# Kernel optimization log

Hardware: AMD Instinct MI355X
Metric: run time of the kernel (lower is better)

## Reference

```python
import jax, jax.numpy as jnp
import numpy as np

N_NODES = 50000
N_EDGES = 800000
FEAT = 128
HID = 64
N_CLS = 12


def setup_inputs() -> dict:
    key = jax.random.key(0)
    ks = jax.random.split(key, 8)
    x = jax.random.normal(ks[0], (N_NODES, FEAT), dtype=jnp.float32)
    edge_index = jax.random.randint(ks[1], (2, N_EDGES), 0, N_NODES, dtype=jnp.int64)
    s1 = 1.0 / np.sqrt(FEAT)
    s2 = 1.0 / np.sqrt(HID)
    W1 = jax.random.uniform(ks[2], (FEAT, HID), jnp.float32, -s1, s1)
    b1 = jnp.zeros((HID,), jnp.float32)
    W2 = jax.random.uniform(ks[3], (HID, HID), jnp.float32, -s2, s2)
    b2 = jnp.zeros((HID,), jnp.float32)
    Wfc = jax.random.uniform(ks[4], (HID, N_CLS), jnp.float32, -s2, s2)
    bfc = jax.random.uniform(ks[5], (N_CLS,), jnp.float32, -s2, s2)
    return {"x": x, "edge_index": edge_index, "W1": W1, "b1": b1,
            "W2": W2, "b2": b2, "Wfc": Wfc, "bfc": bfc}


def gcn_conv(x, W, b, src, dst, n_nodes):
    """PyG GCNConv: symmetric-normalized aggregation with self-loops.
    out_i = sum_{j in N(i)} (xW)_j / sqrt(d_i d_j) + (xW)_i / d_i + b,
    where d = in-degree + 1 (self loop)."""
    xw = x @ W  # [N, out] -- transform before propagate (PyG order)
    deg = jnp.zeros((n_nodes,), x.dtype).at[dst].add(1.0) + 1.0
    dinv = jax.lax.rsqrt(deg)
    norm = dinv[src] * dinv[dst]  # [E]
    agg = jax.ops.segment_sum(xw[src] * norm[:, None], dst, num_segments=n_nodes)
    agg = agg + xw * (dinv * dinv)[:, None]  # self-loop term
    return agg + b


def reference(x, edge_index, W1, b1, W2, b2, Wfc, bfc):
    n = x.shape[0]
    src, dst = edge_index[0], edge_index[1]
    h = jax.nn.relu(gcn_conv(x, W1, b1, src, dst, n))
    h = jax.nn.relu(gcn_conv(h, W2, b2, src, dst, n))
    return h @ Wfc + bfc  # [N, num_content_categories]
```

## Files before the change

kernel.cpp:

```cpp
#include <hip/hip_runtime.h>
#include <hip/hip_fp16.h>


#define CAP   64
#define NBUK  196
#define ET    4096
#define BCAP  5120

typedef unsigned short u16;
typedef unsigned long long u64;
typedef _Float16 f16;
typedef _Float16 f16x8 __attribute__((ext_vector_type(8)));
typedef float f32x4 __attribute__((ext_vector_type(4)));

__global__ __launch_bounds__(256) void k_prep(const float* __restrict__ W1,
                                              const float* __restrict__ W2,
                                              f16* __restrict__ W1t,
                                              f16* __restrict__ W2t,
                                              int* __restrict__ gcur) {
    int i = blockIdx.x * 256 + threadIdx.x;
    if (i < NBUK) gcur[i] = 0;
    if (i < 128 * 64) {
        int k = i >> 6, nn = i & 63;
        W1t[nn * 128 + k] = (f16)W1[k * 64 + nn];
    }
    int j = i - 128 * 64;
    if (j >= 0 && j < 64 * 64) {
        int k = j >> 6, nn = j & 63;
        W2t[nn * 64 + k] = (f16)W2[k * 64 + nn];
    }
}

__global__ __launch_bounds__(256) void k_scat(const int* __restrict__ src,
                                              const int* __restrict__ dst,
                                              int* __restrict__ gcur,
                                              unsigned* __restrict__ eb, int E) {
    __shared__ int hist[NBUK];
    __shared__ int cur[NBUK];
    const int tid = threadIdx.x, blk = blockIdx.x;
    for (int i = tid; i < NBUK; i += 256) hist[i] = 0;
    __syncthreads();

    const int e0 = blk * ET;
    unsigned pk[16];
    if (e0 + ET <= E) {
        const int4* s4 = (const int4*)(src + e0);
        const int4* d4 = (const int4*)(dst + e0);
#pragma unroll
        for (int j = 0; j < ET / 1024; j++) {
            int4 sv = s4[j * 256 + tid];
            int4 dv = d4[j * 256 + tid];
            pk[4 * j + 0] = ((unsigned)dv.x << 16) | (unsigned)sv.x;
            pk[4 * j + 1] = ((unsigned)dv.y << 16) | (unsigned)sv.y;
            pk[4 * j + 2] = ((unsigned)dv.z << 16) | (unsigned)sv.z;
            pk[4 * j + 3] = ((unsigned)dv.w << 16) | (unsigned)sv.w;
            atomicAdd(&hist[(unsigned)dv.x >> 8], 1);
            atomicAdd(&hist[(unsigned)dv.y >> 8], 1);
            atomicAdd(&hist[(unsigned)dv.z >> 8], 1);
            atomicAdd(&hist[(unsigned)dv.w >> 8], 1);
        }
    } else {
#pragma unroll
        for (int j = 0; j < ET / 256; j++) {
            int e = e0 + j * 256 + tid;
            unsigned u = 0xffffffffu;
            if (e < E) {
                unsigned d = (unsigned)dst[e];
                u = (d << 16) | (unsigned)src[e];
                atomicAdd(&hist[d >> 8], 1);
            }
            pk[j] = u;
        }
    }
    __syncthreads();
    for (int b = tid; b < NBUK; b += 256)
        cur[b] = b * BCAP + atomicAdd(&gcur[b], hist[b]);
    __syncthreads();
#pragma unroll
    for (int j = 0; j < 16; j++) {
        unsigned u = pk[j];
        if (u != 0xffffffffu) eb[atomicAdd(&cur[u >> 24], 1)] = u;
    }
}

__global__ __launch_bounds__(1024) void k_buildb(const unsigned* __restrict__ eb,
                                                 const int* __restrict__ gcur,
                                                 u16* __restrict__ csr,
                                                 int* __restrict__ cnt, int n) {
    __shared__ u16 lcsr[256 * CAP];
    __shared__ int cur[256];
    const int tid = threadIdx.x, b = blockIdx.x;
    if (tid < 256) cur[tid] = 0;
    __syncthreads();
    const int e0 = b * BCAP, e1 = e0 + gcur[b];
    for (int e = e0 + tid; e < e1; e += 1024) {
        unsigned u = __builtin_nontemporal_load(eb + e);
        int ld = (int)((u >> 16) & 255u);
        int p = atomicAdd(&cur[ld], 1);
        if (p < CAP) lcsr[ld * CAP + p] = (u16)(u & 0xffffu);
    }
    __syncthreads();
    const int node0 = b * 256;
    for (int i = tid; i < 256 * CAP / 8; i += 1024) {
        int r = i / (CAP / 8), q = i % (CAP / 8);
        int c = cur[r] < CAP ? cur[r] : CAP;
        uint4 v = *(uint4*)&lcsr[r * CAP + q * 8];
        if (q * 8 >= c) v = make_uint4(0, 0, 0, 0);
        *(uint4*)&csr[(size_t)(node0 + r) * CAP + q * 8] = v;
    }
    if (tid < 256 && node0 + tid < n) cnt[node0 + tid] = cur[tid];
}

template <int K, bool IS_HALF, typename TIN>
__global__ __launch_bounds__(256) void k_gemm(const TIN* __restrict__ X,
                                              const f16* __restrict__ Wt,
                                              const int* __restrict__ cnt,
                                              __half* __restrict__ Y, int n) {
    constexpr int KS = K + 8;
    __shared__ f16 xsh[64 * KS];
    __shared__ f16 wsh[64 * KS];
    const int tid = threadIdx.x;
    const int row0 = blockIdx.x * 64;

    for (int i = tid; i < 64 * (K / 8); i += 256) {
        int nn = i / (K / 8), kq = i % (K / 8);
        *(uint4*)&wsh[nn * KS + 8 * kq] = *(const uint4*)&Wt[nn * K + 8 * kq];
    }
    if constexpr (IS_HALF) {
        const __half* Xh = (const __half*)X;
        for (int i = tid; i < 64 * (K / 8); i += 256) {
            int r = i / (K / 8), kq = i % (K / 8);
            uint4 u = make_uint4(0, 0, 0, 0);
            int row = row0 + r;
            if (row < n) u = *(const uint4*)&Xh[(size_t)row * K + 8 * kq];
            *(uint4*)&xsh[r * KS + 8 * kq] = u;
        }
    } else {
        const float* Xf = (const float*)X;
        for (int i = tid; i < 64 * (K / 4); i += 256) {
            int r = i / (K / 4), q4 = i % (K / 4);
            float4 v = make_float4(0.f, 0.f, 0.f, 0.f);
            int row = row0 + r;
            if (row < n) v = *(const float4*)&Xf[(size_t)row * K + 4 * q4];
            __half2 p0 = __floats2half2_rn(v.x, v.y);
            __half2 p1 = __floats2half2_rn(v.z, v.w);
            uint2 o = make_uint2(*(unsigned*)&p0, *(unsigned*)&p1);
            *(uint2*)&xsh[r * KS + 4 * q4] = o;
        }
    }
    __syncthreads();

    const int wv = tid >> 6;
    const int lane = tid & 63;
    const int mn = lane & 15;
    const int q = lane >> 4;

    f32x4 acc[4] = {{0, 0, 0, 0}, {0, 0, 0, 0}, {0, 0, 0, 0}, {0, 0, 0, 0}};
    const f16* arow = &xsh[(16 * wv + mn) * KS + 8 * q];
#pragma unroll
    for (int s = 0; s < K / 32; s++) {
        f16x8 A = *(const f16x8*)&arow[32 * s];
#pragma unroll
        for (int c = 0; c < 4; c++) {
            f16x8 B = *(const f16x8*)&wsh[(16 * c + mn) * KS + 32 * s + 8 * q];
            acc[c] = __builtin_amdgcn_mfma_f32_16x16x32_f16(A, B, acc[c], 0, 0, 0);
        }
    }

    const int rowb = row0 + 16 * wv + 4 * q;
    float dinv[4];
#pragma unroll
    for (int r = 0; r < 4; r++)
        dinv[r] = rsqrtf((float)((rowb + r < n) ? cnt[rowb + r] : 0) + 1.0f);
#pragma unroll
    for (int c = 0; c < 4; c++)
#pragma unroll
        for (int r = 0; r < 4; r++) {
            int row = rowb + r;
            if (row < n)
                Y[(size_t)row * 64 + 16 * c + mn] = __float2half(acc[c][r] * dinv[r]);
        }
}

__device__ __forceinline__ float4 gather_node(const __half* __restrict__ y,
                                              const u16* __restrict__ lst,
                                              int deg, int c4) {
    float4 a0 = make_float4(0.f, 0.f, 0.f, 0.f);
    float4 a1 = make_float4(0.f, 0.f, 0.f, 0.f);
    int i = 0;
    for (; i + 16 <= deg; i += 16) {
        const u64* lp = (const u64*)(lst + i);
        u64 q0 = __builtin_nontemporal_load(lp);
        u64 q1 = __builtin_nontemporal_load(lp + 1);
        u64 q2 = __builtin_nontemporal_load(lp + 2);
        u64 q3 = __builtin_nontemporal_load(lp + 3);
        unsigned idx[16];
#pragma unroll
        for (int t = 0; t < 4; t++) {
            idx[t]      = (unsigned)((q0 >> (16 * t)) & 0xffffu);
            idx[t + 4]  = (unsigned)((q1 >> (16 * t)) & 0xffffu);
            idx[t + 8]  = (unsigned)((q2 >> (16 * t)) & 0xffffu);
            idx[t + 12] = (unsigned)((q3 >> (16 * t)) & 0xffffu);
        }
        uint2 v[16];
#pragma unroll
        for (int t = 0; t < 16; t++) v[t] = *(const uint2*)&y[(size_t)idx[t] * 64 + 4 * c4];
#pragma unroll
        for (int t = 0; t < 16; t += 2) {
            float2 lo0 = __half22float2(*(__half2*)&v[t].x);
            float2 hi0 = __half22float2(*(__half2*)&v[t].y);
            float2 lo1 = __half22float2(*(__half2*)&v[t + 1].x);
            float2 hi1 = __half22float2(*(__half2*)&v[t + 1].y);
            a0.x += lo0.x; a0.y += lo0.y; a0.z += hi0.x; a0.w += hi0.y;
            a1.x += lo1.x; a1.y += lo1.y; a1.z += hi1.x; a1.w += hi1.y;
        }
    }
    if (i + 8 <= deg) {
        const u64* lp = (const u64*)(lst + i);
        u64 q0 = __builtin_nontemporal_load(lp);
        u64 q1 = __builtin_nontemporal_load(lp + 1);
        unsigned idx[8];
#pragma unroll
        for (int t = 0; t < 4; t++) {
            idx[t]     = (unsigned)((q0 >> (16 * t)) & 0xffffu);
            idx[t + 4] = (unsigned)((q1 >> (16 * t)) & 0xffffu);
        }
        uint2 v[8];
#pragma unroll
        for (int t = 0; t < 8; t++) v[t] = *(const uint2*)&y[(size_t)idx[t] * 64 + 4 * c4];
#pragma unroll
        for (int t = 0; t < 8; t += 2) {
            float2 lo0 = __half22float2(*(__half2*)&v[t].x);
            float2 hi0 = __half22float2(*(__half2*)&v[t].y);
            float2 lo1 = __half22float2(*(__half2*)&v[t + 1].x);
            float2 hi1 = __half22float2(*(__half2*)&v[t + 1].y);
            a0.x += lo0.x; a0.y += lo0.y; a0.z += hi0.x; a0.w += hi0.y;
            a1.x += lo1.x; a1.y += lo1.y; a1.z += hi1.x; a1.w += hi1.y;
        }
        i += 8;
    }
    if (i + 4 <= deg) {
        u64 q0 = __builtin_nontemporal_load((const u64*)(lst + i));
        unsigned idx[4];
#pragma unroll
        for (int t = 0; t < 4; t++) idx[t] = (unsigned)((q0 >> (16 * t)) & 0xffffu);
        uint2 v[4];
#pragma unroll
        for (int t = 0; t < 4; t++) v[t] = *(const uint2*)&y[(size_t)idx[t] * 64 + 4 * c4];
#pragma unroll
        for (int t = 0; t < 4; t += 2) {
            float2 lo0 = __half22float2(*(__half2*)&v[t].x);
            float2 hi0 = __half22float2(*(__half2*)&v[t].y);
            float2 lo1 = __half22float2(*(__half2*)&v[t + 1].x);
            float2 hi1 = __half22float2(*(__half2*)&v[t + 1].y);
            a0.x += lo0.x; a0.y += lo0.y; a0.z += hi0.x; a0.w += hi0.y;
            a1.x += lo1.x; a1.y += lo1.y; a1.z += hi1.x; a1.w += hi1.y;
        }
        i += 4;
    }
    for (; i < deg; i++) {
        uint2 vv = *(const uint2*)&y[(size_t)lst[i] * 64 + 4 * c4];
        float2 lo = __half22float2(*(__half2*)&vv.x);
        float2 hi = __half22float2(*(__half2*)&vv.y);
        a0.x += lo.x; a0.y += lo.y; a0.z += hi.x; a0.w += hi.y;
    }
    return make_float4(a0.x + a1.x, a0.y + a1.y, a0.z + a1.z, a0.w + a1.w);
}

__global__ __launch_bounds__(256) void k_agg1(const __half* __restrict__ y,
                                              const u16* __restrict__ csr,
                                              const int* __restrict__ cnt,
                                              const float* __restrict__ bias,
                                              __half* __restrict__ h1, int n) {
    const int tid = threadIdx.x;
    const int c4 = tid & 15;
    const int node = blockIdx.x * 16 + (tid >> 4);
    if (node >= n) return;
    int deg_raw = cnt[node];
    int deg = deg_raw > CAP ? CAP : deg_raw;
    float4 acc = gather_node(y, csr + node * CAP, deg, c4);
    uint2 sv = *(const uint2*)&y[(size_t)node * 64 + 4 * c4];
    float2 slo = __half22float2(*(__half2*)&sv.x);
    float2 shi = __half22float2(*(__half2*)&sv.y);
    float d = rsqrtf((float)deg_raw + 1.0f);
    float4 bv = *(const float4*)&bias[4 * c4];
    float v0 = fmaxf(fmaf(d, acc.x + slo.x, bv.x), 0.f);
    float v1 = fmaxf(fmaf(d, acc.y + slo.y, bv.y), 0.f);
    float v2 = fmaxf(fmaf(d, acc.z + shi.x, bv.z), 0.f);
    float v3 = fmaxf(fmaf(d, acc.w + shi.y, bv.w), 0.f);
    __half2 o0 = __floats2half2_rn(v0, v1);
    __half2 o1 = __floats2half2_rn(v2, v3);
    u64 packed = (u64)(*(unsigned*)&o0) | ((u64)(*(unsigned*)&o1) << 32);
    __builtin_nontemporal_store(packed, (u64*)&h1[(size_t)node * 64 + 4 * c4]);
}

__global__ __launch_bounds__(256) void k_agg2fc(const __half* __restrict__ y,
                                                const u16* __restrict__ csr,
                                                const int* __restrict__ cnt,
                                                const float* __restrict__ bias,
                                                const float* __restrict__ Wfc,
                                                const float* __restrict__ bfc,
                                                float* __restrict__ out, int n) {
    __shared__ float wf[12 * 64];
    __shared__ float bf[12];
    const int tid = threadIdx.x;
    for (int i = tid; i < 12 * 64; i += 256) {
        int c = i >> 6, k = i & 63;
        wf[i] = Wfc[k * 12 + c];
    }
    if (tid < 12) bf[tid] = bfc[tid];
    __syncthreads();

    const int c4 = tid & 15;
    const int node = blockIdx.x * 16 + (tid >> 4);
    if (node >= n) return;
    int deg_raw = cnt[node];
    int deg = deg_raw > CAP ? CAP : deg_raw;
    float4 acc = gather_node(y, csr + node * CAP, deg, c4);
    uint2 sv = *(const uint2*)&y[(size_t)node * 64 + 4 * c4];
    float2 slo = __half22float2(*(__half2*)&sv.x);
    float2 shi = __half22float2(*(__half2*)&sv.y);
    float d = rsqrtf((float)deg_raw + 1.0f);
    float4 bv = *(const float4*)&bias[4 * c4];
    float v0 = fmaxf(fmaf(d, acc.x + slo.x, bv.x), 0.f);
    float v1 = fmaxf(fmaf(d, acc.y + slo.y, bv.y), 0.f);
    float v2 = fmaxf(fmaf(d, acc.z + shi.x, bv.z), 0.f);
    float v3 = fmaxf(fmaf(d, acc.w + shi.y, bv.w), 0.f);

    float res = 0.f;
#pragma unroll
    for (int c = 0; c < 12; c++) {
        float4 wv = *(const float4*)&wf[c * 64 + 4 * c4];
        float p = v0 * wv.x + v1 * wv.y + v2 * wv.z + v3 * wv.w;
        p += __shfl_xor(p, 1);
        p += __shfl_xor(p, 2);
        p += __shfl_xor(p, 4);
        p += __shfl_xor(p, 8);
        if (c4 == c) res = p + bf[c];
    }
    if (c4 < 12) out[(size_t)node * 12 + c4] = res;
}

extern "C" void kernel_launch(void* const* d_in, const int* in_sizes, int n_in,
                              void* d_out, int out_size, void* d_ws, size_t ws_size,
                              hipStream_t stream) {
    const float* x   = (const float*)d_in[0];
    const int*   ei  = (const int*)d_in[1];
    const float* W1  = (const float*)d_in[2];
    const float* b1  = (const float*)d_in[3];
    const float* W2  = (const float*)d_in[4];
    const float* b2  = (const float*)d_in[5];
    const float* Wfc = (const float*)d_in[6];
    const float* bfc = (const float*)d_in[7];
    float* out = (float*)d_out;

    const int n = in_sizes[0] / 128;
    const int E = in_sizes[1] / 2;
    const int* src = ei;
    const int* dst = ei + E;
    const int nblk = (E + ET - 1) / ET;

    char* w = (char*)d_ws;
    unsigned* eb  = (unsigned*)w;  w += (size_t)NBUK * BCAP * 4;
    int* gcur     = (int*)w;       w += 256 * 4;
    int* cnt      = (int*)w;       w += (size_t)((n + 63) / 64) * 64 * 4;
    f16* W1t      = (f16*)w;       w += 128 * 64 * 2;
    f16* W2t      = (f16*)w;       w += 64 * 64 * 2 + 256;
    u16* csr      = (u16*)w;       w += (size_t)NBUK * 256 * CAP * 2;
    __half* y     = (__half*)w;    w += (size_t)n * 64 * 2;
    __half* h1    = (__half*)w;

    k_prep   <<<dim3(48), dim3(256), 0, stream>>>(W1, W2, W1t, W2t, gcur);
    k_scat   <<<dim3(nblk), dim3(256), 0, stream>>>(src, dst, gcur, eb, E);
    k_buildb <<<dim3(NBUK), dim3(1024), 0, stream>>>(eb, gcur, csr, cnt, n);
    k_gemm<128, false, float><<<dim3((n + 63) / 64), dim3(256), 0, stream>>>(x, W1t, cnt, y, n);
    k_agg1   <<<dim3((n + 15) / 16), dim3(256), 0, stream>>>(y, csr, cnt, b1, h1, n);
    k_gemm<64, true, __half><<<dim3((n + 63) / 64), dim3(256), 0, stream>>>(h1, W2t, cnt, y, n);
    k_agg2fc <<<dim3((n + 15) / 16), dim3(256), 0, stream>>>(y, csr, cnt, b2, Wfc, bfc, out, n);
}
```

Baseline: 164.6 us.

## Fuse layer-1 aggregation with layer-2 GEMM via per-block MFMA

Merges the first aggregation kernel and the second dense transform into one kernel. Each block aggregates 16 nodes into shared memory, then uses MFMA 16x16x32 f16 instructions against W2 staged in LDS to produce the scaled layer-2 features directly. This removes the h1 intermediate write/read round trip and one kernel launch. In exchange, every block reloads W2 into LDS, uses more shared memory, and adds a block-wide barrier that could lower occupancy.

```diff
diff --git a/kernel.cpp b/kernel.cpp
--- a/kernel.cpp
+++ b/kernel.cpp
@@ -267,12 +267,84 @@
     return make_float4(a0.x + a1.x, a0.y + a1.y, a0.z + a1.z, a0.w + a1.w);
 }
 
-__global__ __launch_bounds__(256) void k_agg1(const __half* __restrict__ y,
-                                              const u16* __restrict__ csr,
-                                              const int* __restrict__ cnt,
-                                              const float* __restrict__ bias,
-                                              __half* __restrict__ h1, int n) {
+__global__ __launch_bounds__(256) void k_agg1g2(const __half* __restrict__ y,
+                                                const u16* __restrict__ csr,
+                                                const int* __restrict__ cnt,
+                                                const float* __restrict__ bias,
+                                                const f16* __restrict__ W2t,
+                                                __half* __restrict__ y2, int n) {
+    constexpr int KS2 = 64 + 8;
+    __shared__ f16 ash[16 * KS2];
+    __shared__ f16 wsh[64 * KS2];
+    __shared__ float dsh[16];
     const int tid = threadIdx.x;
+    const int node0 = blockIdx.x * 16;
+
+    for (int i = tid; i < 64 * 8; i += 256) {
+        int nn = i >> 3, kq = i & 7;
+        *(uint4*)&wsh[nn * KS2 + 8 * kq] = *(const uint4*)&W2t[nn * 64 + 8 * kq];
+    }
+
+    const int c4 = tid & 15;
+    const int r16 = tid >> 4;
+    const int node = node0 + r16;
+    const int nodeC = node < n ? node : 0;
+    int deg_raw = (node < n) ? cnt[node] : 0;
+    int deg = deg_raw > CAP ? CAP : deg_raw;
+    float4 acc = gather_node(y, csr + (size_t)nodeC * CAP, deg, c4);
+    uint2 sv = *(const uint2*)&y[(size_t)nodeC * 64 + 4 * c4];
+    float2 slo = __half22float2(*(__half2*)&sv.x);
+    float2 shi = __half22float2(*(__half2*)&sv.y);
+    float d = rsqrtf((float)deg_raw + 1.0f);
+    float4 bv = *(const float4*)&bias[4 * c4];
+    float v0 = fmaxf(fmaf(d, acc.x + slo.x, bv.x), 0.f);
+    float v1 = fmaxf(fmaf(d, acc.y + slo.y, bv.y), 0.f);
+    float v2 = fmaxf(fmaf(d, acc.z + shi.x, bv.z), 0.f);
+    float v3 = fmaxf(fmaf(d, acc.w + shi.y, bv.w), 0.f);
+    __half2 o0 = __floats2half2_rn(v0, v1);
+    __half2 o1 = __floats2half2_rn(v2, v3);
+    u64 packed = (u64)(*(unsigned*)&o0) | ((u64)(*(unsigned*)&o1) << 32);
+    *(u64*)&ash[r16 * KS2 + 4 * c4] = packed;
+    if (c4 == 0) dsh[r16] = d;
+    __syncthreads();
+
+    const int wv = tid >> 6;
+    const int lane = tid & 63;
+    const int mn = lane & 15;
+    const int q = lane >> 4;
+    f32x4 acc2 = {0, 0, 0, 0};
+#pragma unroll
+    for (int s = 0; s < 2; s++) {
+        f16x8 A = *(const f16x8*)&ash[mn * KS2 + 32 * s + 8 * q];
+        f16x8 B = *(const f16x8*)&wsh[(16 * wv + mn) * KS2 + 32 * s + 8 * q];
+        acc2 = __builtin_amdgcn_mfma_f32_16x16x32_f16(A, B, acc2, 0, 0, 0);
+    }
+#pragma unroll
+    for (int r = 0; r < 4; r++) {
+        int row = node0 + 4 * q + r;
+        if (row < n)
+            y2[(size_t)row * 64 + 16 * wv + mn] =
+                __float2half(acc2[r] * dsh[4 * q + r]);
+    }
+}
+
+__global__ __launch_bounds__(256) void k_agg2fc(const __half* __restrict__ y,
+                                                const u16* __restrict__ csr,
+                                                const int* __restrict__ cnt,
+                                                const float* __restrict__ bias,
+                                                const float* __restrict__ Wfc,
+                                                const float* __restrict__ bfc,
+                                                float* __restrict__ out, int n) {
+    __shared__ float wf[12 * 64];
+    __shared__ float bf[12];
+    const int tid = threadIdx.x;
+    for (int i = tid; i < 12 * 64; i += 256) {
+        int c = i >> 6, k = i & 63;
+        wf[i] = Wfc[k * 12 + c];
+    }
+    if (tid < 12) bf[tid] = bfc[tid];
+    __syncthreads();
+
     const int c4 = tid & 15;
     const int node = blockIdx.x * 16 + (tid >> 4);
     if (node >= n) return;
@@ -288,44 +360,6 @@
     float v1 = fmaxf(fmaf(d, acc.y + slo.y, bv.y), 0.f);
     float v2 = fmaxf(fmaf(d, acc.z + shi.x, bv.z), 0.f);
     float v3 = fmaxf(fmaf(d, acc.w + shi.y, bv.w), 0.f);
-    __half2 o0 = __floats2half2_rn(v0, v1);
-    __half2 o1 = __floats2half2_rn(v2, v3);
-    u64 packed = (u64)(*(unsigned*)&o0) | ((u64)(*(unsigned*)&o1) << 32);
-    __builtin_nontemporal_store(packed, (u64*)&h1[(size_t)node * 64 + 4 * c4]);
-}
-
-__global__ __launch_bounds__(256) void k_agg2fc(const __half* __restrict__ y,
-                                                const u16* __restrict__ csr,
-                                                const int* __restrict__ cnt,
-                                                const float* __restrict__ bias,
-                                                const float* __restrict__ Wfc,
-                                                const float* __restrict__ bfc,
-                                                float* __restrict__ out, int n) {
-    __shared__ float wf[12 * 64];
-    __shared__ float bf[12];
-    const int tid = threadIdx.x;
-    for (int i = tid; i < 12 * 64; i += 256) {
-        int c = i >> 6, k = i & 63;
-        wf[i] = Wfc[k * 12 + c];
-    }
-    if (tid < 12) bf[tid] = bfc[tid];
-    __syncthreads();
-
-    const int c4 = tid & 15;
-    const int node = blockIdx.x * 16 + (tid >> 4);
-    if (node >= n) return;
-    int deg_raw = cnt[node];
-    int deg = deg_raw > CAP ? CAP : deg_raw;
-    float4 acc = gather_node(y, csr + node * CAP, deg, c4);
-    uint2 sv = *(const uint2*)&y[(size_t)node * 64 + 4 * c4];
-    float2 slo = __half22float2(*(__half2*)&sv.x);
-    float2 shi = __half22float2(*(__half2*)&sv.y);
-    float d = rsqrtf((float)deg_raw + 1.0f);
-    float4 bv = *(const float4*)&bias[4 * c4];
-    float v0 = fmaxf(fmaf(d, acc.x + slo.x, bv.x), 0.f);
-    float v1 = fmaxf(fmaf(d, acc.y + slo.y, bv.y), 0.f);
-    float v2 = fmaxf(fmaf(d, acc.z + shi.x, bv.z), 0.f);
-    float v3 = fmaxf(fmaf(d, acc.w + shi.y, bv.w), 0.f);
 
     float res = 0.f;
 #pragma unroll
@@ -368,13 +402,12 @@
     f16* W2t      = (f16*)w;       w += 64 * 64 * 2 + 256;
     u16* csr      = (u16*)w;       w += (size_t)NBUK * 256 * CAP * 2;
     __half* y     = (__half*)w;    w += (size_t)n * 64 * 2;
-    __half* h1    = (__half*)w;
+    __half* y2    = (__half*)w;
 
     k_prep   <<<dim3(48), dim3(256), 0, stream>>>(W1, W2, W1t, W2t, gcur);
     k_scat   <<<dim3(nblk), dim3(256), 0, stream>>>(src, dst, gcur, eb, E);
     k_buildb <<<dim3(NBUK), dim3(1024), 0, stream>>>(eb, gcur, csr, cnt, n);
     k_gemm<128, false, float><<<dim3((n + 63) / 64), dim3(256), 0, stream>>>(x, W1t, cnt, y, n);
-    k_agg1   <<<dim3((n + 15) / 16), dim3(256), 0, stream>>>(y, csr, cnt, b1, h1, n);
-    k_gemm<64, true, __half><<<dim3((n + 63) / 64), dim3(256), 0, stream>>>(h1, W2t, cnt, y, n);
-    k_agg2fc <<<dim3((n + 15) / 16), dim3(256), 0, stream>>>(y, csr, cnt, b2, Wfc, bfc, out, n);
-}
+    k_agg1g2 <<<dim3((n + 15) / 16), dim3(256), 0, stream>>>(y, csr, cnt, b1, W2t, y2, n);
+    k_agg2fc <<<dim3((n + 15) / 16), dim3(256), 0, stream>>>(y2, csr, cnt, b2, Wfc, bfc, out, n);
+}
```

Measured after the change: 156.7 us. 1.05x faster.
